# Performance work log

Measured on AMD Instinct MI355X. Metric: run time of the kernel, lower is better.

The kernel has to match this reference:

```python
import jax, jax.numpy as jnp
import numpy as np

N = 20000      # nodes
E = 640000     # edges
F_IN = 256     # num_features
HID = 256      # hidden_dim
EMB = 256      # embedding_dim
OUT = 1        # output_dim


def setup_inputs() -> dict:
    key = jax.random.key(0)
    ks = jax.random.split(key, 8)
    g = lambda k, shp: jax.random.normal(k, shp, dtype=jnp.float32) / np.sqrt(shp[0]).astype(np.float32)
    return {
        "x": jax.random.normal(ks[0], (N, F_IN), dtype=jnp.float32),
        "edge_index": jax.random.randint(ks[1], (2, E), 0, N, dtype=jnp.int64),
        "W1": g(ks[2], (F_IN, HID)),
        "b1": jnp.zeros((HID,), jnp.float32),
        "Wh": g(ks[3], (HID, HID)),
        "bh": jnp.zeros((HID,), jnp.float32),
        "W2": g(ks[4], (HID, EMB)),
        "b2": jnp.zeros((EMB,), jnp.float32),
        "Wout": g(ks[5], (EMB, OUT)),
        "bout": jnp.zeros((OUT,), jnp.float32),
    }


def reference(x, edge_index, W1, b1, Wh, bh, W2, b2, Wout, bout):
    n = x.shape[0]
    # PyG GCNConv: add self-loops, symmetric normalization D^-1/2 (A+I) D^-1/2
    loop = jnp.arange(n, dtype=edge_index.dtype)
    row = jnp.concatenate([edge_index[0], loop])  # source j
    col = jnp.concatenate([edge_index[1], loop])  # target i
    deg = jax.ops.segment_sum(jnp.ones(row.shape[0], x.dtype), col, num_segments=n)
    dinv = jnp.where(deg > 0, jax.lax.rsqrt(deg), 0.0)
    norm = dinv[row] * dinv[col]  # [E+N]

    def conv(h, W, b):
        hw = h @ W                                   # dense GEMM [n, d_out]
        msg = hw[row] * norm[:, None]                # gather + scale
        return jax.ops.segment_sum(msg, col, num_segments=n) + b  # scatter-add

    h = jax.nn.relu(conv(x, W1, b1))   # gcn1 (dropout_rate=0 -> identity)
    h = jax.nn.relu(conv(h, Wh, bh))   # hidden GCNConv
    h = conv(h, W2, b2)                # gcn2 -> embedding
    out = h @ Wout + bout              # Decoder_linear
    return (out, h)
```

## Files before the change

kernel.cpp:

```cpp
#include <hip/hip_runtime.h>
#include <hip/hip_bf16.h>

#define NN 20000
#define EE 640000

typedef __attribute__((ext_vector_type(8))) short bf16x8;
typedef __attribute__((ext_vector_type(4))) float f32x4;

__device__ __forceinline__ ushort f2b(float f) {
    __hip_bfloat16 h = __float2bfloat16(f);
    return *(ushort*)&h;
}
__device__ __forceinline__ float b2f(ushort u) {
    __hip_bfloat16 h = *(__hip_bfloat16*)&u;
    return __bfloat162float(h);
}

__device__ __forceinline__ void acc8(float m, bf16x8 v, float* acc) {
    union { bf16x8 v; unsigned u[4]; } t;
    t.v = v;
    #pragma unroll
    for (int k = 0; k < 4; ++k) {
        acc[2 * k]     = fmaf(m, __uint_as_float(t.u[k] << 16), acc[2 * k]);
        acc[2 * k + 1] = fmaf(m, __uint_as_float(t.u[k] & 0xffff0000u), acc[2 * k + 1]);
    }
}

__device__ __forceinline__ void gload16(const ushort* g, ushort* l) {
    __builtin_amdgcn_global_load_lds(
        (const __attribute__((address_space(1))) void*)g,
        (__attribute__((address_space(3))) void*)l, 16, 0, 0);
}


__global__ void init_cnt_kernel(int* __restrict__ cnt, int n) {
    int i = blockIdx.x * 256 + threadIdx.x;
    if (i < n) cnt[i] = 0;
}

__global__ void hist_kernel(const int* __restrict__ col, int* __restrict__ cnt, int e) {
    int i = blockIdx.x * 256 + threadIdx.x;
    if (i < e) atomicAdd(&cnt[col[i]], 1);
}

__device__ __forceinline__ int block_exscan(int v) {
    __shared__ int wsum[4];
    int tid = threadIdx.x, lane = tid & 63, w = tid >> 6;
    int x = v;
    #pragma unroll
    for (int d = 1; d < 64; d <<= 1) {
        int y = __shfl_up(x, d, 64);
        if (lane >= d) x += y;
    }
    if (lane == 63) wsum[w] = x;
    __syncthreads();
    if (tid == 0) {
        int s = 0;
        #pragma unroll
        for (int k = 0; k < 4; ++k) { int t = wsum[k]; wsum[k] = s; s += t; }
    }
    __syncthreads();
    return wsum[w] + x - v;
}

__global__ __launch_bounds__(256) void scan_p1_kernel(const int* __restrict__ cnt,
                                                      int* __restrict__ offs,
                                                      int* __restrict__ bsum,
                                                      float* __restrict__ dinv, int n) {
    int i = blockIdx.x * 256 + threadIdx.x;
    int v = (i < n) ? cnt[i] : 0;
    int e = block_exscan(v);
    if (i < n) {
        offs[i] = e;
        dinv[i] = rsqrtf((float)(v + 1));
    }
    if (threadIdx.x == 255) bsum[blockIdx.x] = e + v;
}

__global__ __launch_bounds__(256) void scan_p2_kernel(int* __restrict__ bsum, int nblk) {
    int t = threadIdx.x;
    int v = (t < nblk) ? bsum[t] : 0;
    int e = block_exscan(v);
    if (t < nblk) bsum[t] = e;
}

__global__ __launch_bounds__(256) void scan_p3_kernel(int* __restrict__ offs,
                                                      const int* __restrict__ bsum,
                                                      int* __restrict__ cursor, int n) {
    int i = blockIdx.x * 256 + threadIdx.x;
    if (i < n) {
        int o = offs[i] + bsum[blockIdx.x];
        offs[i] = o;
        cursor[i] = o;
    }
}

__global__ void scatter_kernel(const int* __restrict__ row, const int* __restrict__ col,
                               const float* __restrict__ dinv, int* __restrict__ cursor,
                               unsigned* __restrict__ pq, int e) {
    int i = blockIdx.x * 256 + threadIdx.x;
    if (i >= e) return;
    int s = row[i], d = col[i];
    int pos = atomicAdd(&cursor[d], 1);
    unsigned nb = f2b(dinv[s] * dinv[d]);
    pq[pos] = (nb << 16) | (unsigned)s;
}

__global__ __launch_bounds__(256) void cvt_kernel(const float* __restrict__ x,
                                                  ushort* __restrict__ xb, int total8) {
    int i = blockIdx.x * 256 + threadIdx.x;
    if (i >= total8) return;
    float4 a = ((const float4*)x)[2 * i];
    float4 b = ((const float4*)x)[2 * i + 1];
    union { bf16x8 v; ushort s[8]; } o;
    o.s[0] = f2b(a.x); o.s[1] = f2b(a.y); o.s[2] = f2b(a.z); o.s[3] = f2b(a.w);
    o.s[4] = f2b(b.x); o.s[5] = f2b(b.y); o.s[6] = f2b(b.z); o.s[7] = f2b(b.w);
    ((bf16x8*)xb)[i] = o.v;
}

__global__ __launch_bounds__(256) void wprep_kernel(const float* __restrict__ W1,
                                                    const float* __restrict__ Wh,
                                                    const float* __restrict__ W2,
                                                    ushort* __restrict__ Wt) {
    const float* W = (blockIdx.y == 0) ? W1 : ((blockIdx.y == 1) ? Wh : W2);
    ushort* dst = Wt + (size_t)blockIdx.y * 256 * 768;
    int col = blockIdx.x;
    for (int kv = threadIdx.x; kv < 768; kv += 256) {
        int k = kv & 255;
        float w = W[(size_t)k * 256 + col];
        ushort hi = f2b(w);
        ushort out = (kv < 256 || kv >= 512) ? hi : f2b(w - b2f(hi));
        dst[(size_t)col * 768 + kv] = out;
    }
}

__global__ __launch_bounds__(256) void agg_kernel(
    const ushort* __restrict__ hb,
    const int* __restrict__ offs, const int* __restrict__ cnt,
    const unsigned* __restrict__ pq,
    const float* __restrict__ dinv,
    ushort* __restrict__ a2, int n) {
    int chunk = blockIdx.x & 3;
    int lane = threadIdx.x & 63;
    int half = lane >> 5;
    int esub = (lane >> 3) & 3;
    int fsub = lane & 7;
    int node = (blockIdx.x >> 2) * 8 + (threadIdx.x >> 6) * 2 + half;
    const ushort* base = hb + chunk * 64 + fsub * 8;

    int beg = offs[node], num = cnt[node];
    float acc[8] = {};

    int e0 = esub, e1 = 4 + esub, e2 = 8 + esub, e3 = 12 + esub;
    unsigned q0 = pq[e0 < num ? beg + e0 : 0];
    unsigned q1 = pq[e1 < num ? beg + e1 : 0];
    unsigned q2 = pq[e2 < num ? beg + e2 : 0];
    unsigned q3 = pq[e3 < num ? beg + e3 : 0];

    for (int j = 0; j < num; j += 16) {
        int jn = j + 16;
        int k0 = jn + esub, k1 = jn + 4 + esub, k2 = jn + 8 + esub, k3 = jn + 12 + esub;
        unsigned p0 = pq[k0 < num ? beg + k0 : 0];
        unsigned p1 = pq[k1 < num ? beg + k1 : 0];
        unsigned p2 = pq[k2 < num ? beg + k2 : 0];
        unsigned p3 = pq[k3 < num ? beg + k3 : 0];

        float m0 = (j +      esub) < num ? __uint_as_float(q0 & 0xffff0000u) : 0.f;
        float m1 = (j + 4  + esub) < num ? __uint_as_float(q1 & 0xffff0000u) : 0.f;
        float m2 = (j + 8  + esub) < num ? __uint_as_float(q2 & 0xffff0000u) : 0.f;
        float m3 = (j + 12 + esub) < num ? __uint_as_float(q3 & 0xffff0000u) : 0.f;
        bf16x8 v0 = *(const bf16x8*)(base + (size_t)(q0 & 0xffffu) * 256);
        bf16x8 v1 = *(const bf16x8*)(base + (size_t)(q1 & 0xffffu) * 256);
        bf16x8 v2 = *(const bf16x8*)(base + (size_t)(q2 & 0xffffu) * 256);
        bf16x8 v3 = *(const bf16x8*)(base + (size_t)(q3 & 0xffffu) * 256);
        acc8(m0, v0, acc);
        acc8(m1, v1, acc);
        acc8(m2, v2, acc);
        acc8(m3, v3, acc);
        q0 = p0; q1 = p1; q2 = p2; q3 = p3;
    }

    #pragma unroll
    for (int d = 8; d < 32; d <<= 1)
        #pragma unroll
        for (int k = 0; k < 8; ++k)
            acc[k] += __shfl_xor(acc[k], d, 64);

    if (esub == 0) {
        float di = dinv[node];
        bf16x8 sv = *(const bf16x8*)(base + (size_t)node * 256);
        acc8(di * di, sv, acc);
        int feat = chunk * 64 + fsub * 8;
        union { bf16x8 v; ushort s[8]; } hi, lo;
        #pragma unroll
        for (int k = 0; k < 8; ++k) {
            unsigned u = __float_as_uint(acc[k]);
            hi.s[k] = (ushort)(u >> 16);
            float l = acc[k] - __uint_as_float(u & 0xffff0000u);
            lo.s[k] = (ushort)(__float_as_uint(l) >> 16);
        }
        *(bf16x8*)(a2 + (size_t)node * 512 + feat)       = hi.v;
        *(bf16x8*)(a2 + (size_t)node * 512 + 256 + feat) = lo.v;
    }
}

__global__ void init_out_kernel(float* __restrict__ out, const float* __restrict__ bout, int n) {
    int i = blockIdx.x * 256 + threadIdx.x;
    if (i < n) out[i] = bout[0];
}

template<bool RELU, bool BF16OUT, bool FUSE>
__global__ __launch_bounds__(256) void gemm_mfma_kernel(
    const ushort* __restrict__ A2, const ushort* __restrict__ Wt,
    const float* __restrict__ bias, void* __restrict__ Cout,
    const float* __restrict__ Wout, float* __restrict__ outv, int n) {
    __shared__ ushort Ast[2][128][64];
    __shared__ ushort Bst[2][64][64];
    int tid = threadIdx.x;
    int lane = tid & 63, wid = tid >> 6;
    int rowbase = blockIdx.x * 128;
    int colbase = blockIdx.y * 64;

    f32x4 zero = {0.f, 0.f, 0.f, 0.f};
    f32x4 acc[2][4];
    #pragma unroll
    for (int m = 0; m < 2; ++m)
        #pragma unroll
        for (int nn = 0; nn < 4; ++nn) acc[m][nn] = zero;

    int rsub = lane >> 3, sl = lane & 7;
    const ushort* asrc[4];
    #pragma unroll
    for (int q = 0; q < 4; ++q) {
        int rin = wid * 32 + q * 8 + rsub;
        int c = sl ^ (rin & 7);
        int gr = min(rowbase + rin, n - 1);
        asrc[q] = A2 + (size_t)gr * 512 + c * 8;
    }
    const ushort* bsrc[2];
    #pragma unroll
    for (int q = 0; q < 2; ++q) {
        int rin = wid * 16 + q * 8 + rsub;
        int c = sl ^ (rin & 7);
        bsrc[q] = Wt + (size_t)(colbase + rin) * 768 + c * 8;
    }

    auto stage = [&](int kt, int buf) {
        int kv0 = kt * 64;
        int acol0 = (kv0 < 256) ? kv0 : kv0 - 256;
        #pragma unroll
        for (int q = 0; q < 4; ++q)
            gload16(asrc[q] + acol0, &Ast[buf][wid * 32 + q * 8][0]);
        #pragma unroll
        for (int q = 0; q < 2; ++q)
            gload16(bsrc[q] + kv0, &Bst[buf][wid * 16 + q * 8][0]);
    };

    stage(0, 0);
    for (int kt = 0; kt < 12; ++kt) {
        int cur = kt & 1;
        if (kt < 11) {
            stage(kt + 1, cur ^ 1);
            asm volatile("s_waitcnt vmcnt(6)" ::: "memory");
        } else {
            asm volatile("s_waitcnt vmcnt(0)" ::: "memory");
        }
        __builtin_amdgcn_s_barrier();
        #pragma unroll
        for (int kk = 0; kk < 2; ++kk) {
            int clog = kk * 4 + (lane >> 4);
            bf16x8 af[2], bf[4];
            #pragma unroll
            for (int m = 0; m < 2; ++m) {
                int row = wid * 32 + m * 16 + (lane & 15);
                af[m] = *(const bf16x8*)&Ast[cur][row][(clog ^ (row & 7)) * 8];
            }
            #pragma unroll
            for (int nn = 0; nn < 4; ++nn) {
                int row = nn * 16 + (lane & 15);
                bf[nn] = *(const bf16x8*)&Bst[cur][row][(clog ^ (row & 7)) * 8];
            }
            #pragma unroll
            for (int m = 0; m < 2; ++m)
                #pragma unroll
                for (int nn = 0; nn < 4; ++nn)
                    acc[m][nn] = __builtin_amdgcn_mfma_f32_16x16x32_bf16(
                        af[m], bf[nn], acc[m][nn], 0, 0, 0);
        }
        __builtin_amdgcn_s_barrier();
    }

    float rowdot[2][4] = {};
    #pragma unroll
    for (int nn = 0; nn < 4; ++nn) {
        int col = colbase + nn * 16 + (lane & 15);
        float bv = bias[col];
        float wv = FUSE ? Wout[col] : 0.f;
        #pragma unroll
        for (int m = 0; m < 2; ++m) {
            int grow0 = rowbase + wid * 32 + m * 16 + ((lane >> 4) << 2);
            f32x4 v = acc[m][nn];
            #pragma unroll
            for (int rr = 0; rr < 4; ++rr) {
                int row = grow0 + rr;
                if (row < n) {
                    float val = v[rr] + bv;
                    if (RELU) val = fmaxf(val, 0.f);
                    if (BF16OUT)
                        ((ushort*)Cout)[(size_t)row * 256 + col] = f2b(val);
                    else
                        ((float*)Cout)[(size_t)row * 256 + col] = val;
                    if (FUSE) rowdot[m][rr] = fmaf(val, wv, rowdot[m][rr]);
                }
            }
        }
    }
    if (FUSE) {
        #pragma unroll
        for (int m = 0; m < 2; ++m)
            #pragma unroll
            for (int rr = 0; rr < 4; ++rr) {
                float v = rowdot[m][rr];
                #pragma unroll
                for (int d = 1; d < 16; d <<= 1)
                    v += __shfl_xor(v, d, 64);
                if ((lane & 15) == 0) {
                    int row = rowbase + wid * 32 + m * 16 + ((lane >> 4) << 2) + rr;
                    if (row < n) atomicAdd(&outv[row], v);
                }
            }
    }
}

extern "C" void kernel_launch(void* const* d_in, const int* in_sizes, int n_in,
                              void* d_out, int out_size, void* d_ws, size_t ws_size,
                              hipStream_t stream) {
    const int n = NN, e = EE;
    const float* x    = (const float*)d_in[0];
    const int*   eidx = (const int*)d_in[1];
    const float* W1   = (const float*)d_in[2];
    const float* b1   = (const float*)d_in[3];
    const float* Wh   = (const float*)d_in[4];
    const float* bh   = (const float*)d_in[5];
    const float* W2   = (const float*)d_in[6];
    const float* b2   = (const float*)d_in[7];
    const float* Wout = (const float*)d_in[8];
    const float* bout = (const float*)d_in[9];
    const int* row = eidx;
    const int* col = eidx + e;

    char* ws = (char*)d_ws;
    int*      cnt     = (int*)ws;      ws += (size_t)n * 4;
    int*      offs    = (int*)ws;      ws += (size_t)n * 4;
    int*      cursor  = (int*)ws;      ws += (size_t)n * 4;
    float*    dinv    = (float*)ws;    ws += (size_t)n * 4;
    int*      bsum    = (int*)ws;      ws += (size_t)256 * 4;
    unsigned* pq      = (unsigned*)ws; ws += (size_t)e * 4;
    ushort*   hb      = (ushort*)ws;   ws += (size_t)n * 256 * 2;
    ushort*   a2      = (ushort*)ws;   ws += (size_t)n * 512 * 2;
    ushort*   wt      = (ushort*)ws;   ws += (size_t)3 * 256 * 768 * 2;
    ushort* wt1 = wt;
    ushort* wt2 = wt + (size_t)256 * 768;
    ushort* wt3 = wt + (size_t)2 * 256 * 768;

    float* outv = (float*)d_out;
    float* h3   = (float*)d_out + n;

    int nb_n = (n + 255) / 256;
    int nb_e = (e + 255) / 256;

    init_cnt_kernel<<<nb_n, 256, 0, stream>>>(cnt, n);
    hist_kernel<<<nb_e, 256, 0, stream>>>(col, cnt, e);
    scan_p1_kernel<<<nb_n, 256, 0, stream>>>(cnt, offs, bsum, dinv, n);
    scan_p2_kernel<<<1, 256, 0, stream>>>(bsum, nb_n);
    scan_p3_kernel<<<nb_n, 256, 0, stream>>>(offs, bsum, cursor, n);
    scatter_kernel<<<nb_e, 256, 0, stream>>>(row, col, dinv, cursor, pq, e);

    wprep_kernel<<<dim3(256, 3), 256, 0, stream>>>(W1, Wh, W2, wt);
    cvt_kernel<<<(n * 32 + 255) / 256, 256, 0, stream>>>(x, hb, n * 32);
    init_out_kernel<<<nb_n, 256, 0, stream>>>(outv, bout, n);

    int agrid = (n / 8) * 4;
    dim3 ggrid((n + 127) / 128, 4);

    agg_kernel<<<agrid, 256, 0, stream>>>(hb, offs, cnt, pq, dinv, a2, n);
    gemm_mfma_kernel<true, true, false><<<ggrid, 256, 0, stream>>>(
        a2, wt1, b1, hb, nullptr, nullptr, n);
    agg_kernel<<<agrid, 256, 0, stream>>>(hb, offs, cnt, pq, dinv, a2, n);
    gemm_mfma_kernel<true, true, false><<<ggrid, 256, 0, stream>>>(
        a2, wt2, bh, hb, nullptr, nullptr, n);
    agg_kernel<<<agrid, 256, 0, stream>>>(hb, offs, cnt, pq, dinv, a2, n);
    gemm_mfma_kernel<false, false, true><<<ggrid, 256, 0, stream>>>(
        a2, wt3, b2, h3, Wout, outv, n);
}
```

Measured before the change: 255.9 us.

## Reorder GCN layers to GEMM-then-aggregate and drop split-precision A operand

Each layer now runs the dense GEMM first (A·W computed as h@W) and then aggregates the bf16 result over neighbours, applying bias, ReLU, the final decoder dot and the output writes in the aggregation epilogue. The A operand is now plain bf16 (K=512 instead of 768 in the hi/lo scheme), cutting GEMM work and the A2 buffer size. The three prep kernels are merged into one launch. In exchange the GEMM output is rounded to bf16 before aggregation, which removes the lo-part compensation on activations and may increase numerical error.

```diff
diff --git a/kernel.cpp b/kernel.cpp
--- a/kernel.cpp
+++ b/kernel.cpp
@@ -106,64 +106,168 @@
     pq[pos] = (nb << 16) | (unsigned)s;
 }
 
-__global__ __launch_bounds__(256) void cvt_kernel(const float* __restrict__ x,
-                                                  ushort* __restrict__ xb, int total8) {
-    int i = blockIdx.x * 256 + threadIdx.x;
-    if (i >= total8) return;
-    float4 a = ((const float4*)x)[2 * i];
-    float4 b = ((const float4*)x)[2 * i + 1];
-    union { bf16x8 v; ushort s[8]; } o;
-    o.s[0] = f2b(a.x); o.s[1] = f2b(a.y); o.s[2] = f2b(a.z); o.s[3] = f2b(a.w);
-    o.s[4] = f2b(b.x); o.s[5] = f2b(b.y); o.s[6] = f2b(b.z); o.s[7] = f2b(b.w);
-    ((bf16x8*)xb)[i] = o.v;
-}
-
-__global__ __launch_bounds__(256) void wprep_kernel(const float* __restrict__ W1,
-                                                    const float* __restrict__ Wh,
-                                                    const float* __restrict__ W2,
-                                                    ushort* __restrict__ Wt) {
-    const float* W = (blockIdx.y == 0) ? W1 : ((blockIdx.y == 1) ? Wh : W2);
-    ushort* dst = Wt + (size_t)blockIdx.y * 256 * 768;
-    int col = blockIdx.x;
-    for (int kv = threadIdx.x; kv < 768; kv += 256) {
-        int k = kv & 255;
-        float w = W[(size_t)k * 256 + col];
-        ushort hi = f2b(w);
-        ushort out = (kv < 256 || kv >= 512) ? hi : f2b(w - b2f(hi));
-        dst[(size_t)col * 768 + kv] = out;
-    }
-}
-
+__global__ __launch_bounds__(256) void prep_kernel(
+    const float* __restrict__ W1, const float* __restrict__ Wh,
+    const float* __restrict__ W2, ushort* __restrict__ Wt,
+    const float* __restrict__ x, ushort* __restrict__ xb,
+    const float* __restrict__ bout, float* __restrict__ outv, int n) {
+    int bid = blockIdx.x;
+    if (bid < 768) {
+        const float* W = (bid < 256) ? W1 : ((bid < 512) ? Wh : W2);
+        ushort* dst = Wt + (size_t)(bid >> 8) * 256 * 512;
+        int col = bid & 255;
+        #pragma unroll
+        for (int kv = threadIdx.x; kv < 512; kv += 256) {
+            int k = kv & 255;
+            float w = W[(size_t)k * 256 + col];
+            ushort hi = f2b(w);
+            dst[(size_t)col * 512 + kv] = (kv < 256) ? hi : f2b(w - b2f(hi));
+        }
+    } else if (bid < 768 + 2500) {
+        int i = (bid - 768) * 256 + threadIdx.x;
+        if (i < n * 32) {
+            float4 a = ((const float4*)x)[2 * i];
+            float4 b = ((const float4*)x)[2 * i + 1];
+            union { bf16x8 v; ushort s[8]; } o;
+            o.s[0] = f2b(a.x); o.s[1] = f2b(a.y); o.s[2] = f2b(a.z); o.s[3] = f2b(a.w);
+            o.s[4] = f2b(b.x); o.s[5] = f2b(b.y); o.s[6] = f2b(b.z); o.s[7] = f2b(b.w);
+            ((bf16x8*)xb)[i] = o.v;
+        }
+    } else {
+        int i = (bid - 3268) * 256 + threadIdx.x;
+        if (i < n) outv[i] = bout[0];
+    }
+}
+
+__global__ __launch_bounds__(256) void gemm_mfma_kernel(
+    const ushort* __restrict__ A, const ushort* __restrict__ Wt,
+    ushort* __restrict__ G, int n) {
+    __shared__ ushort Ast[2][128][64];
+    __shared__ ushort Bst[2][64][64];
+    int tid = threadIdx.x;
+    int lane = tid & 63, wid = tid >> 6;
+    int rowbase = blockIdx.x * 128;
+    int colbase = blockIdx.y * 64;
+
+    f32x4 zero = {0.f, 0.f, 0.f, 0.f};
+    f32x4 acc[2][4];
+    #pragma unroll
+    for (int m = 0; m < 2; ++m)
+        #pragma unroll
+        for (int nn = 0; nn < 4; ++nn) acc[m][nn] = zero;
+
+    int rsub = lane >> 3, sl = lane & 7;
+    const ushort* asrc[4];
+    #pragma unroll
+    for (int q = 0; q < 4; ++q) {
+        int rin = wid * 32 + q * 8 + rsub;
+        int c = sl ^ (rin & 7);
+        int gr = min(rowbase + rin, n - 1);
+        asrc[q] = A + (size_t)gr * 256 + c * 8;
+    }
+    const ushort* bsrc[2];
+    #pragma unroll
+    for (int q = 0; q < 2; ++q) {
+        int rin = wid * 16 + q * 8 + rsub;
+        int c = sl ^ (rin & 7);
+        bsrc[q] = Wt + (size_t)(colbase + rin) * 512 + c * 8;
+    }
+
+    auto stage = [&](int kt, int buf) {
+        int kv0 = kt * 64;
+        int acol0 = kv0 & 255;
+        #pragma unroll
+        for (int q = 0; q < 4; ++q)
+            gload16(asrc[q] + acol0, &Ast[buf][wid * 32 + q * 8][0]);
+        #pragma unroll
+        for (int q = 0; q < 2; ++q)
+            gload16(bsrc[q] + kv0, &Bst[buf][wid * 16 + q * 8][0]);
+    };
+
+    stage(0, 0);
+    for (int kt = 0; kt < 8; ++kt) {
+        int cur = kt & 1;
+        if (kt < 7) {
+            stage(kt + 1, cur ^ 1);
+            asm volatile("s_waitcnt vmcnt(6)" ::: "memory");
+        } else {
+            asm volatile("s_waitcnt vmcnt(0)" ::: "memory");
+        }
+        __builtin_amdgcn_s_barrier();
+        #pragma unroll
+        for (int kk = 0; kk < 2; ++kk) {
+            int clog = kk * 4 + (lane >> 4);
+            bf16x8 af[2], bf[4];
+            #pragma unroll
+            for (int m = 0; m < 2; ++m) {
+                int row = wid * 32 + m * 16 + (lane & 15);
+                af[m] = *(const bf16x8*)&Ast[cur][row][(clog ^ (row & 7)) * 8];
+            }
+            #pragma unroll
+            for (int nn = 0; nn < 4; ++nn) {
+                int row = nn * 16 + (lane & 15);
+                bf[nn] = *(const bf16x8*)&Bst[cur][row][(clog ^ (row & 7)) * 8];
+            }
+            #pragma unroll
+            for (int m = 0; m < 2; ++m)
+                #pragma unroll
+                for (int nn = 0; nn < 4; ++nn)
+                    acc[m][nn] = __builtin_amdgcn_mfma_f32_16x16x32_bf16(
+                        af[m], bf[nn], acc[m][nn], 0, 0, 0);
+        }
+        __builtin_amdgcn_s_barrier();
+    }
+
+    #pragma unroll
+    for (int nn = 0; nn < 4; ++nn) {
+        int col = colbase + nn * 16 + (lane & 15);
+        #pragma unroll
+        for (int m = 0; m < 2; ++m) {
+            int grow0 = rowbase + wid * 32 + m * 16 + ((lane >> 4) << 2);
+            f32x4 v = acc[m][nn];
+            #pragma unroll
+            for (int rr = 0; rr < 4; ++rr) {
+                int row = grow0 + rr;
+                if (row < n)
+                    G[(size_t)row * 256 + col] = f2b(v[rr]);
+            }
+        }
+    }
+}
+
+template<bool FINAL>
 __global__ __launch_bounds__(256) void agg_kernel(
-    const ushort* __restrict__ hb,
+    const ushort* __restrict__ g,
     const int* __restrict__ offs, const int* __restrict__ cnt,
     const unsigned* __restrict__ pq,
     const float* __restrict__ dinv,
-    ushort* __restrict__ a2, int n) {
+    const float* __restrict__ bias,
+    ushort* __restrict__ hb,
+    float* __restrict__ h3,
+    const float* __restrict__ Wout, float* __restrict__ outv,
+    int n) {
     int chunk = blockIdx.x & 3;
     int lane = threadIdx.x & 63;
     int half = lane >> 5;
     int esub = (lane >> 3) & 3;
     int fsub = lane & 7;
     int node = (blockIdx.x >> 2) * 8 + (threadIdx.x >> 6) * 2 + half;
-    const ushort* base = hb + chunk * 64 + fsub * 8;
+    const ushort* base = g + chunk * 64 + fsub * 8;
 
     int beg = offs[node], num = cnt[node];
     float acc[8] = {};
 
-    int e0 = esub, e1 = 4 + esub, e2 = 8 + esub, e3 = 12 + esub;
-    unsigned q0 = pq[e0 < num ? beg + e0 : 0];
-    unsigned q1 = pq[e1 < num ? beg + e1 : 0];
-    unsigned q2 = pq[e2 < num ? beg + e2 : 0];
-    unsigned q3 = pq[e3 < num ? beg + e3 : 0];
+    unsigned q0 = pq[(esub)      < num ? beg + esub      : 0];
+    unsigned q1 = pq[(4 + esub)  < num ? beg + 4 + esub  : 0];
+    unsigned q2 = pq[(8 + esub)  < num ? beg + 8 + esub  : 0];
+    unsigned q3 = pq[(12 + esub) < num ? beg + 12 + esub : 0];
 
     for (int j = 0; j < num; j += 16) {
         int jn = j + 16;
-        int k0 = jn + esub, k1 = jn + 4 + esub, k2 = jn + 8 + esub, k3 = jn + 12 + esub;
-        unsigned p0 = pq[k0 < num ? beg + k0 : 0];
-        unsigned p1 = pq[k1 < num ? beg + k1 : 0];
-        unsigned p2 = pq[k2 < num ? beg + k2 : 0];
-        unsigned p3 = pq[k3 < num ? beg + k3 : 0];
+        unsigned p0 = pq[(jn + esub)      < num ? beg + jn + esub      : 0];
+        unsigned p1 = pq[(jn + 4 + esub)  < num ? beg + jn + 4 + esub  : 0];
+        unsigned p2 = pq[(jn + 8 + esub)  < num ? beg + jn + 8 + esub  : 0];
+        unsigned p3 = pq[(jn + 12 + esub) < num ? beg + jn + 12 + esub : 0];
 
         float m0 = (j +      esub) < num ? __uint_as_float(q0 & 0xffff0000u) : 0.f;
         float m1 = (j + 4  + esub) < num ? __uint_as_float(q1 & 0xffff0000u) : 0.f;
@@ -191,144 +295,30 @@
         bf16x8 sv = *(const bf16x8*)(base + (size_t)node * 256);
         acc8(di * di, sv, acc);
         int feat = chunk * 64 + fsub * 8;
-        union { bf16x8 v; ushort s[8]; } hi, lo;
-        #pragma unroll
-        for (int k = 0; k < 8; ++k) {
-            unsigned u = __float_as_uint(acc[k]);
-            hi.s[k] = (ushort)(u >> 16);
-            float l = acc[k] - __uint_as_float(u & 0xffff0000u);
-            lo.s[k] = (ushort)(__float_as_uint(l) >> 16);
-        }
-        *(bf16x8*)(a2 + (size_t)node * 512 + feat)       = hi.v;
-        *(bf16x8*)(a2 + (size_t)node * 512 + 256 + feat) = lo.v;
-    }
-}
-
-__global__ void init_out_kernel(float* __restrict__ out, const float* __restrict__ bout, int n) {
-    int i = blockIdx.x * 256 + threadIdx.x;
-    if (i < n) out[i] = bout[0];
-}
-
-template<bool RELU, bool BF16OUT, bool FUSE>
-__global__ __launch_bounds__(256) void gemm_mfma_kernel(
-    const ushort* __restrict__ A2, const ushort* __restrict__ Wt,
-    const float* __restrict__ bias, void* __restrict__ Cout,
-    const float* __restrict__ Wout, float* __restrict__ outv, int n) {
-    __shared__ ushort Ast[2][128][64];
-    __shared__ ushort Bst[2][64][64];
-    int tid = threadIdx.x;
-    int lane = tid & 63, wid = tid >> 6;
-    int rowbase = blockIdx.x * 128;
-    int colbase = blockIdx.y * 64;
-
-    f32x4 zero = {0.f, 0.f, 0.f, 0.f};
-    f32x4 acc[2][4];
-    #pragma unroll
-    for (int m = 0; m < 2; ++m)
-        #pragma unroll
-        for (int nn = 0; nn < 4; ++nn) acc[m][nn] = zero;
-
-    int rsub = lane >> 3, sl = lane & 7;
-    const ushort* asrc[4];
-    #pragma unroll
-    for (int q = 0; q < 4; ++q) {
-        int rin = wid * 32 + q * 8 + rsub;
-        int c = sl ^ (rin & 7);
-        int gr = min(rowbase + rin, n - 1);
-        asrc[q] = A2 + (size_t)gr * 512 + c * 8;
-    }
-    const ushort* bsrc[2];
-    #pragma unroll
-    for (int q = 0; q < 2; ++q) {
-        int rin = wid * 16 + q * 8 + rsub;
-        int c = sl ^ (rin & 7);
-        bsrc[q] = Wt + (size_t)(colbase + rin) * 768 + c * 8;
-    }
-
-    auto stage = [&](int kt, int buf) {
-        int kv0 = kt * 64;
-        int acol0 = (kv0 < 256) ? kv0 : kv0 - 256;
-        #pragma unroll
-        for (int q = 0; q < 4; ++q)
-            gload16(asrc[q] + acol0, &Ast[buf][wid * 32 + q * 8][0]);
-        #pragma unroll
-        for (int q = 0; q < 2; ++q)
-            gload16(bsrc[q] + kv0, &Bst[buf][wid * 16 + q * 8][0]);
-    };
-
-    stage(0, 0);
-    for (int kt = 0; kt < 12; ++kt) {
-        int cur = kt & 1;
-        if (kt < 11) {
-            stage(kt + 1, cur ^ 1);
-            asm volatile("s_waitcnt vmcnt(6)" ::: "memory");
+        float4 b0 = *(const float4*)(bias + feat);
+        float4 b1 = *(const float4*)(bias + feat + 4);
+        acc[0] += b0.x; acc[1] += b0.y; acc[2] += b0.z; acc[3] += b0.w;
+        acc[4] += b1.x; acc[5] += b1.y; acc[6] += b1.z; acc[7] += b1.w;
+        if (!FINAL) {
+            union { bf16x8 v; ushort s[8]; } o;
+            #pragma unroll
+            for (int k = 0; k < 8; ++k)
+                o.s[k] = f2b(fmaxf(acc[k], 0.f));
+            *(bf16x8*)(hb + (size_t)node * 256 + feat) = o.v;
         } else {
-            asm volatile("s_waitcnt vmcnt(0)" ::: "memory");
-        }
-        __builtin_amdgcn_s_barrier();
-        #pragma unroll
-        for (int kk = 0; kk < 2; ++kk) {
-            int clog = kk * 4 + (lane >> 4);
-            bf16x8 af[2], bf[4];
-            #pragma unroll
-            for (int m = 0; m < 2; ++m) {
-                int row = wid * 32 + m * 16 + (lane & 15);
-                af[m] = *(const bf16x8*)&Ast[cur][row][(clog ^ (row & 7)) * 8];
-            }
-            #pragma unroll
-            for (int nn = 0; nn < 4; ++nn) {
-                int row = nn * 16 + (lane & 15);
-                bf[nn] = *(const bf16x8*)&Bst[cur][row][(clog ^ (row & 7)) * 8];
-            }
-            #pragma unroll
-            for (int m = 0; m < 2; ++m)
-                #pragma unroll
-                for (int nn = 0; nn < 4; ++nn)
-                    acc[m][nn] = __builtin_amdgcn_mfma_f32_16x16x32_bf16(
-                        af[m], bf[nn], acc[m][nn], 0, 0, 0);
-        }
-        __builtin_amdgcn_s_barrier();
-    }
-
-    float rowdot[2][4] = {};
-    #pragma unroll
-    for (int nn = 0; nn < 4; ++nn) {
-        int col = colbase + nn * 16 + (lane & 15);
-        float bv = bias[col];
-        float wv = FUSE ? Wout[col] : 0.f;
-        #pragma unroll
-        for (int m = 0; m < 2; ++m) {
-            int grow0 = rowbase + wid * 32 + m * 16 + ((lane >> 4) << 2);
-            f32x4 v = acc[m][nn];
-            #pragma unroll
-            for (int rr = 0; rr < 4; ++rr) {
-                int row = grow0 + rr;
-                if (row < n) {
-                    float val = v[rr] + bv;
-                    if (RELU) val = fmaxf(val, 0.f);
-                    if (BF16OUT)
-                        ((ushort*)Cout)[(size_t)row * 256 + col] = f2b(val);
-                    else
-                        ((float*)Cout)[(size_t)row * 256 + col] = val;
-                    if (FUSE) rowdot[m][rr] = fmaf(val, wv, rowdot[m][rr]);
-                }
-            }
-        }
-    }
-    if (FUSE) {
-        #pragma unroll
-        for (int m = 0; m < 2; ++m)
-            #pragma unroll
-            for (int rr = 0; rr < 4; ++rr) {
-                float v = rowdot[m][rr];
-                #pragma unroll
-                for (int d = 1; d < 16; d <<= 1)
-                    v += __shfl_xor(v, d, 64);
-                if ((lane & 15) == 0) {
-                    int row = rowbase + wid * 32 + m * 16 + ((lane >> 4) << 2) + rr;
-                    if (row < n) atomicAdd(&outv[row], v);
-                }
-            }
+            float4 o0 = {acc[0], acc[1], acc[2], acc[3]};
+            float4 o1 = {acc[4], acc[5], acc[6], acc[7]};
+            *(float4*)(h3 + (size_t)node * 256 + feat)     = o0;
+            *(float4*)(h3 + (size_t)node * 256 + feat + 4) = o1;
+            float4 w0 = *(const float4*)(Wout + feat);
+            float4 w1 = *(const float4*)(Wout + feat + 4);
+            float dot = acc[0] * w0.x + acc[1] * w0.y + acc[2] * w0.z + acc[3] * w0.w
+                      + acc[4] * w1.x + acc[5] * w1.y + acc[6] * w1.z + acc[7] * w1.w;
+            #pragma unroll
+            for (int d = 1; d < 8; d <<= 1)
+                dot += __shfl_xor(dot, d, 64);
+            if (fsub == 0) atomicAdd(&outv[node], dot);
+        }
     }
 }
 
@@ -356,12 +346,13 @@
     float*    dinv    = (float*)ws;    ws += (size_t)n * 4;
     int*      bsum    = (int*)ws;      ws += (size_t)256 * 4;
     unsigned* pq      = (unsigned*)ws; ws += (size_t)e * 4;
+    ushort*   xb      = (ushort*)ws;   ws += (size_t)n * 256 * 2;
     ushort*   hb      = (ushort*)ws;   ws += (size_t)n * 256 * 2;
-    ushort*   a2      = (ushort*)ws;   ws += (size_t)n * 512 * 2;
-    ushort*   wt      = (ushort*)ws;   ws += (size_t)3 * 256 * 768 * 2;
+    ushort*   g2      = (ushort*)ws;   ws += (size_t)n * 256 * 2;
+    ushort*   wt      = (ushort*)ws;   ws += (size_t)3 * 256 * 512 * 2;
     ushort* wt1 = wt;
-    ushort* wt2 = wt + (size_t)256 * 768;
-    ushort* wt3 = wt + (size_t)2 * 256 * 768;
+    ushort* wt2 = wt + (size_t)256 * 512;
+    ushort* wt3 = wt + (size_t)2 * 256 * 512;
 
     float* outv = (float*)d_out;
     float* h3   = (float*)d_out + n;
@@ -376,20 +367,18 @@
     scan_p3_kernel<<<nb_n, 256, 0, stream>>>(offs, bsum, cursor, n);
     scatter_kernel<<<nb_e, 256, 0, stream>>>(row, col, dinv, cursor, pq, e);
 
-    wprep_kernel<<<dim3(256, 3), 256, 0, stream>>>(W1, Wh, W2, wt);
-    cvt_kernel<<<(n * 32 + 255) / 256, 256, 0, stream>>>(x, hb, n * 32);
-    init_out_kernel<<<nb_n, 256, 0, stream>>>(outv, bout, n);
+    prep_kernel<<<768 + 2500 + 79, 256, 0, stream>>>(W1, Wh, W2, wt, x, xb, bout, outv, n);
 
     int agrid = (n / 8) * 4;
     dim3 ggrid((n + 127) / 128, 4);
 
-    agg_kernel<<<agrid, 256, 0, stream>>>(hb, offs, cnt, pq, dinv, a2, n);
-    gemm_mfma_kernel<true, true, false><<<ggrid, 256, 0, stream>>>(
-        a2, wt1, b1, hb, nullptr, nullptr, n);
-    agg_kernel<<<agrid, 256, 0, stream>>>(hb, offs, cnt, pq, dinv, a2, n);
-    gemm_mfma_kernel<true, true, false><<<ggrid, 256, 0, stream>>>(
-        a2, wt2, bh, hb, nullptr, nullptr, n);
-    agg_kernel<<<agrid, 256, 0, stream>>>(hb, offs, cnt, pq, dinv, a2, n);
-    gemm_mfma_kernel<false, false, true><<<ggrid, 256, 0, stream>>>(
-        a2, wt3, b2, h3, Wout, outv, n);
-}
+    gemm_mfma_kernel<<<ggrid, 256, 0, stream>>>(xb, wt1, g2, n);
+    agg_kernel<false><<<agrid, 256, 0, stream>>>(
+        g2, offs, cnt, pq, dinv, b1, hb, nullptr, nullptr, nullptr, n);
+    gemm_mfma_kernel<<<ggrid, 256, 0, stream>>>(hb, wt2, g2, n);
+    agg_kernel<false><<<agrid, 256, 0, stream>>>(
+        g2, offs, cnt, pq, dinv, bh, hb, nullptr, nullptr, nullptr, n);
+    gemm_mfma_kernel<<<ggrid, 256, 0, stream>>>(hb, wt3, g2, n);
+    agg_kernel<true><<<agrid, 256, 0, stream>>>(
+        g2, offs, cnt, pq, dinv, b2, nullptr, h3, Wout, outv, n);
+}
```

Result: faster. 223.1 us (-12.8%).
